# Kernel tuning notes

Hardware: AMD Instinct MI355X
Metric: run time of the kernel (lower is better)

The kernel has to match this reference:

```python
import jax, jax.numpy as jnp
import numpy as np

K, M, C, P = 3, 64, 1, 7
EPS = 1e-16


def _conv_c(x, w, transpose=False):
    """Complex 2D conv (stride 1, SAME padding) decomposed into 4 real convs.
    x: complex [B,Cin,H,W]; w: complex torch-layout weight.
    transpose=True emulates nn.ConvTranspose2d(M,C,P,stride=1,padding=(P-1)//2):
    weight layout (in=M, out=C, P, P), spatially flipped kernel.
    """
    xr, xi = jnp.real(x), jnp.imag(x)
    wr, wi = jnp.real(w), jnp.imag(w)
    if transpose:
        wr = jnp.flip(wr, (2, 3))
        wi = jnp.flip(wi, (2, 3))
        dn = ('NCHW', 'IOHW', 'NCHW')
    else:
        dn = ('NCHW', 'OIHW', 'NCHW')
    f = lambda a, b: jax.lax.conv_general_dilated(
        a, b, window_strides=(1, 1), padding='SAME', dimension_numbers=dn)
    return jax.lax.complex(f(xr, wr) - f(xi, wi), f(xr, wi) + f(xi, wr))


def _st_complex(x, t):
    """Complex soft-threshold: x * relu(|x| - t) / (|x| + eps)."""
    a = jnp.abs(x)
    return x * (jax.nn.relu(a - t) / (a + EPS))


def setup_inputs() -> dict:
    key = jax.random.key(0)
    ks = jax.random.split(key, 7)
    B, H, W = 4, 256, 256
    wscale = 1.0 / np.sqrt(2.0 * M * P * P)  # keep unrolled loop stable
    return {
        'y_re': jax.random.normal(ks[0], (B, C, H, W), jnp.float32),
        'y_im': jax.random.normal(ks[1], (B, C, H, W), jnp.float32),
        'Aw_re': jax.random.normal(ks[2], (K, M, C, P, P), jnp.float32) * wscale,
        'Aw_im': jax.random.normal(ks[3], (K, M, C, P, P), jnp.float32) * wscale,
        'Bw_re': jax.random.normal(ks[4], (K, M, C, P, P), jnp.float32) * wscale,
        'Bw_im': jax.random.normal(ks[5], (K, M, C, P, P), jnp.float32) * wscale,
        't': jax.random.uniform(ks[6], (K, 2, M, 1, 1), jnp.float32) * 0.01,
    }


def reference(y_re, y_im, Aw_re, Aw_im, Bw_re, Bw_im, t):
    y = jax.lax.complex(y_re, y_im)
    Aw = jax.lax.complex(Aw_re, Aw_im)   # [K,M,C,P,P], Conv2d weights
    Bw = jax.lax.complex(Bw_re, Bw_im)   # [K,M,C,P,P], ConvTranspose2d weights

    # pre_process (stride=1, mask=1): mean-subtract, no padding
    mean = jnp.mean(y, axis=(1, 2, 3), keepdims=True)
    yp = y - mean

    # _lista_core with sigma=None, adaptive=False => c=0, threshold = t[k,0]
    z = _st_complex(_conv_c(yp, Aw[0]), t[0, 0])  # [B,M,H,W] complex
    for k in range(1, K):
        r = _conv_c(z, Bw[k], transpose=True) - yp  # mask == 1
        z = z - _conv_c(r, Aw[k])
        z = _st_complex(z, t[k, 0])

    # decode: D = B[0]; post_process adds mean back
    xhat = _conv_c(z, Bw[0], transpose=True) + mean
    return xhat, z
```

## Files before the change

### kernel.cpp

```cpp
#include <hip/hip_runtime.h>

#define Hh 256
#define Ww 256
#define NB 4
#define NM 64
#define KP 7
#define HW (Hh*Ww)
#define NX (NB*HW)
#define NZQ ((size_t)NB*NM*HW)
#define PT 32
#define TW2 38
#define LDS2 40
#define NST 6
#define NTAP (3*NM*49)
#define NSPL 4

typedef unsigned short u16;
typedef unsigned int u32;

__device__ __forceinline__ float bf2f(u16 u) {
  union { u32 i; float f; } c; c.i = ((u32)u) << 16; return c.f;
}
__device__ __forceinline__ u16 f2bf(float f) {
  union { float f; u32 i; } c; c.f = f;
  return (u16)((c.i + 0x7FFFu + ((c.i >> 16) & 1u)) >> 16);
}
__device__ __forceinline__ ushort2 packbf(float x, float y) {
  return make_ushort2(f2bf(x), f2bf(y));
}

__device__ __forceinline__ u32 packh(float x, float y) {
  union { u32 u; _Float16 h[2]; } c;
  c.h[0] = (_Float16)x; c.h[1] = (_Float16)y;
  return c.u;
}
__device__ __forceinline__ float2 unpackh(u32 v) {
  union { u32 u; _Float16 h[2]; } c; c.u = v;
  return make_float2((float)c.h[0], (float)c.h[1]);
}
__device__ __forceinline__ u16 h2bf(u16 hraw) {
  union { u16 u; _Float16 h; } c; c.u = hraw;
  return f2bf((float)c.h);
}

#if __has_builtin(__builtin_amdgcn_fdot2)
typedef _Float16 hf2 __attribute__((ext_vector_type(2)));
__device__ __forceinline__ void cmac2(float& ar, float& ai, u32 v, u32 wre, u32 wim) {
  union { u32 u; hf2 h; } a, b, c;
  a.u = v; b.u = wre; c.u = wim;
  ar = __builtin_amdgcn_fdot2(a.h, b.h, ar, false);
  ai = __builtin_amdgcn_fdot2(a.h, c.h, ai, false);
}
#else
__device__ __forceinline__ void cmac2(float& ar, float& ai, u32 v, u32 wre, u32 wim) {
  float2 a = unpackh(v), b = unpackh(wre), c = unpackh(wim);
  ar = fmaf(a.x, b.x, ar); ar = fmaf(a.y, b.y, ar);
  ai = fmaf(a.x, c.x, ai); ai = fmaf(a.y, c.y, ai);
}
#endif

__global__ __launch_bounds__(256) void wprep_kernel(
    const float* __restrict__ Awre, const float* __restrict__ Awim,
    const float* __restrict__ Bwre, const float* __restrict__ Bwim,
    uint2* __restrict__ wA, uint2* __restrict__ wB) {
  int i = blockIdx.x*256 + threadIdx.x;
  if (i < NTAP) {
    float wr = Awre[i], wi = Awim[i];
    wA[i] = make_uint2(packh(wr, -wi), packh(wi, wr));
    wr = Bwre[i]; wi = Bwim[i];
    wB[i] = make_uint2(packh(wr, -wi), packh(wi, wr));
  }
}

__global__ __launch_bounds__(256) void mean_stage1(
    const float* __restrict__ yre, const float* __restrict__ yim,
    float2* __restrict__ part) {
  int blk = blockIdx.x;
  int b = blk >> 6, chunk = blk & 63;
  int tid = threadIdx.x;
  int base = b*HW + chunk*1024;
  float sr = 0.f, si = 0.f;
  #pragma unroll
  for (int j = 0; j < 4; ++j) {
    sr += yre[base + tid + j*256];
    si += yim[base + tid + j*256];
  }
  #pragma unroll
  for (int off = 32; off > 0; off >>= 1) {
    sr += __shfl_down(sr, off);
    si += __shfl_down(si, off);
  }
  __shared__ float2 red[4];
  if ((tid & 63) == 0) red[tid >> 6] = make_float2(sr, si);
  __syncthreads();
  if (tid == 0) {
    float2 a = red[0], b2 = red[1], c = red[2], d = red[3];
    part[blk] = make_float2(a.x + b2.x + c.x + d.x, a.y + b2.y + c.y + d.y);
  }
}

__global__ __launch_bounds__(256) void mean_stage2(
    const float2* __restrict__ part, float2* __restrict__ mean) {
  int tid = threadIdx.x;
  int b = tid >> 6, lane = tid & 63;
  float2 v = part[b*64 + lane];
  float sr = v.x, si = v.y;
  #pragma unroll
  for (int off = 32; off > 0; off >>= 1) {
    sr += __shfl_down(sr, off);
    si += __shfl_down(si, off);
  }
  if (lane == 0) mean[b] = make_float2(sr / (float)HW, si / (float)HW);
}

__global__ __launch_bounds__(256) void conv_first_kernel(
    const float* __restrict__ yre, const float* __restrict__ yim,
    const float2* __restrict__ mean,
    const uint2* __restrict__ wA,
    const float* __restrict__ t, u32* __restrict__ z) {
  int tid = threadIdx.x;
  int blk = blockIdx.x;
  int ms  = blk & 3;
  int txi = (blk >> 2) & 7, tyi = (blk >> 5) & 7, b = (blk >> 8) & 3;
  int ty0 = tyi*PT, tx0 = txi*PT;
  int thy = tid >> 4, thx = tid & 15;

  __shared__ u32 tile[TW2][LDS2];
  float2 mb = mean[b];
  const float* re = yre + b*HW;
  const float* im = yim + b*HW;
  for (int i = tid; i < TW2*TW2; i += 256) {
    int rr = i / TW2, cc = i - rr*TW2;
    int gy = ty0 - 3 + rr, gx = tx0 - 3 + cc;
    u32 v = 0;
    if ((unsigned)gy < Hh && (unsigned)gx < Ww) {
      int o = gy*Ww + gx;
      v = packh(re[o] - mb.x, im[o] - mb.y);
    }
    tile[rr][cc] = v;
  }
  __syncthreads();

  u32* zb = z + ((size_t)b*NM << 16);
  int m0 = ms*16;
  #pragma unroll 1
  for (int mm = 0; mm < 16; mm += 4) {
    int m = m0 + mm;
    const uint2* w0p = wA + m*49;
    float ar[4][4], ai[4][4];
    #pragma unroll
    for (int c = 0; c < 4; ++c)
      #pragma unroll
      for (int p = 0; p < 4; ++p) { ar[c][p] = 0.f; ai[c][p] = 0.f; }
    #pragma unroll
    for (int ky = 0; ky < KP; ++ky) {
      #pragma unroll
      for (int kx = 0; kx < KP; ++kx) {
        int wo = ky*KP + kx;
        uint2 w0 = w0p[wo], w1 = w0p[49 + wo], w2 = w0p[98 + wo], w3 = w0p[147 + wo];
        #pragma unroll
        for (int dy = 0; dy < 2; ++dy) {
          #pragma unroll
          for (int dx = 0; dx < 2; ++dx) {
            u32 v = tile[thy + dy*16 + ky][thx + dx*16 + kx];
            int p = dy*2 + dx;
            cmac2(ar[0][p], ai[0][p], v, w0.x, w0.y);
            cmac2(ar[1][p], ai[1][p], v, w1.x, w1.y);
            cmac2(ar[2][p], ai[2][p], v, w2.x, w2.y);
            cmac2(ar[3][p], ai[3][p], v, w3.x, w3.y);
          }
        }
      }
    }
    #pragma unroll
    for (int c = 0; c < 4; ++c) {
      float tc = t[m + c];
      #pragma unroll
      for (int dy = 0; dy < 2; ++dy) {
        #pragma unroll
        for (int dx = 0; dx < 2; ++dx) {
          int p = dy*2 + dx;
          size_t o = (size_t)(ty0 + thy + dy*16)*Ww + tx0 + thx + dx*16;
          float a0 = sqrtf(ar[c][p]*ar[c][p] + ai[c][p]*ai[c][p]);
          float f0 = fmaxf(a0 - tc, 0.f) / (a0 + 1e-16f);
          zb[((size_t)(m + c) << 16) + o] = packh(ar[c][p]*f0, ai[c][p]*f0);
        }
      }
    }
  }
}

__global__ __launch_bounds__(256) void convT_part_kernel(
    const u32* __restrict__ z,
    const uint2* __restrict__ wB,
    int k, float2* __restrict__ rpart) {
  int tid = threadIdx.x;
  int blk = blockIdx.x;
  int s   = blk & 3;
  int txi = (blk >> 2) & 7, tyi = (blk >> 5) & 7, b = (blk >> 8) & 3;
  int ty0 = tyi*PT, tx0 = txi*PT;
  int thy = tid >> 4, thx = tid & 15;

  __shared__ uint2 tile[TW2][LDS2];

  int srr[NST], scc[NST], soff[NST];
  bool sok[NST], sin[NST];
  #pragma unroll
  for (int j = 0; j < NST; ++j) {
    int i = tid + j*256;
    sin[j] = i < TW2*TW2;
    int rr = sin[j] ? i / TW2 : 0;
    int cc = sin[j] ? i - rr*TW2 : 0;
    int gy = ty0 - 3 + rr, gx = tx0 - 3 + cc;
    sok[j] = sin[j] && (unsigned)gy < Hh && (unsigned)gx < Ww;
    srr[j] = rr; scc[j] = cc;
    soff[j] = sok[j] ? gy*Ww + gx : 0;
  }

  const u32* zb = z + ((size_t)b*NM << 16);
  int m0 = s*16;

  float ar[4] = {0.f,0.f,0.f,0.f}, ai[4] = {0.f,0.f,0.f,0.f};
  #pragma unroll 1
  for (int q = 0; q < 8; ++q) {
    int m = m0 + 2*q;
    if (q) __syncthreads();
    {
      const u32* za = zb + ((size_t)m << 16);
      const u32* zc = zb + ((size_t)(m + 1) << 16);
      #pragma unroll
      for (int j = 0; j < NST; ++j)
        if (sin[j]) tile[srr[j]][scc[j]] =
          make_uint2(sok[j] ? za[soff[j]] : 0u, sok[j] ? zc[soff[j]] : 0u);
    }
    __syncthreads();

    const uint2* w0p = wB + (k*NM + m)*49;
    const uint2* w1p = w0p + 49;
    #pragma unroll
    for (int ky = 0; ky < KP; ++ky) {
      #pragma unroll
      for (int kx = 0; kx < KP; ++kx) {
        int wo = ky*KP + kx;
        uint2 wa = w0p[wo], wb = w1p[wo];
        #pragma unroll
        for (int dy = 0; dy < 2; ++dy) {
          #pragma unroll
          for (int dx = 0; dx < 2; ++dx) {
            uint2 v = tile[thy + dy*16 + 6 - ky][thx + dx*16 + 6 - kx];
            int p = dy*2 + dx;
            cmac2(ar[p], ai[p], v.x, wa.x, wa.y);
            cmac2(ar[p], ai[p], v.y, wb.x, wb.y);
          }
        }
      }
    }
  }

  float2* rp = rpart + (size_t)s*NB*HW + (size_t)b*HW;
  #pragma unroll
  for (int dy = 0; dy < 2; ++dy) {
    #pragma unroll
    for (int dx = 0; dx < 2; ++dx) {
      int p = dy*2 + dx;
      int o = (ty0 + thy + dy*16)*Ww + tx0 + thx + dx*16;
      rp[o] = make_float2(ar[p], ai[p]);
    }
  }
}

__global__ __launch_bounds__(256) void conv_update_kernel(
    const float2* __restrict__ rpart,
    const float* __restrict__ yre, const float* __restrict__ yim,
    const float2* __restrict__ mean,
    const uint2* __restrict__ wA,
    const float* __restrict__ t, int k, u32* __restrict__ z) {
  int tid = threadIdx.x;
  int blk = blockIdx.x;
  int ms  = blk & 3;
  int txi = (blk >> 2) & 7, tyi = (blk >> 5) & 7, b = (blk >> 8) & 3;
  int ty0 = tyi*PT, tx0 = txi*PT;
  int thy = tid >> 4, thx = tid & 15;

  __shared__ u32 tile[TW2][LDS2];
  float2 mb = mean[b];
  for (int i = tid; i < TW2*TW2; i += 256) {
    int rr = i / TW2, cc = i - rr*TW2;
    int gy = ty0 - 3 + rr, gx = tx0 - 3 + cc;
    u32 v = 0;
    if ((unsigned)gy < Hh && (unsigned)gx < Ww) {
      int o = b*HW + gy*Ww + gx;
      float2 p0 = rpart[o];
      float2 p1 = rpart[(size_t)NB*HW + o];
      float2 p2 = rpart[(size_t)2*NB*HW + o];
      float2 p3 = rpart[(size_t)3*NB*HW + o];
      v = packh(p0.x + p1.x + p2.x + p3.x - (yre[o] - mb.x),
                p0.y + p1.y + p2.y + p3.y - (yim[o] - mb.y));
    }
    tile[rr][cc] = v;
  }
  __syncthreads();

  const float* tw = t + k*2*NM;
  u32* zb = z + ((size_t)b*NM << 16);
  int m0 = ms*16;
  #pragma unroll 1
  for (int mm = 0; mm < 16; mm += 4) {
    int m = m0 + mm;
    const uint2* w0p = wA + (k*NM + m)*49;
    float ar[4][4], ai[4][4];
    #pragma unroll
    for (int c = 0; c < 4; ++c)
      #pragma unroll
      for (int p = 0; p < 4; ++p) { ar[c][p] = 0.f; ai[c][p] = 0.f; }
    #pragma unroll
    for (int ky = 0; ky < KP; ++ky) {
      #pragma unroll
      for (int kx = 0; kx < KP; ++kx) {
        int wo = ky*KP + kx;
        uint2 w0 = w0p[wo], w1 = w0p[49 + wo], w2 = w0p[98 + wo], w3 = w0p[147 + wo];
        #pragma unroll
        for (int dy = 0; dy < 2; ++dy) {
          #pragma unroll
          for (int dx = 0; dx < 2; ++dx) {
            u32 v = tile[thy + dy*16 + ky][thx + dx*16 + kx];
            int p = dy*2 + dx;
            cmac2(ar[0][p], ai[0][p], v, w0.x, w0.y);
            cmac2(ar[1][p], ai[1][p], v, w1.x, w1.y);
            cmac2(ar[2][p], ai[2][p], v, w2.x, w2.y);
            cmac2(ar[3][p], ai[3][p], v, w3.x, w3.y);
          }
        }
      }
    }
    #pragma unroll
    for (int c = 0; c < 4; ++c) {
      float tc = tw[m + c];
      #pragma unroll
      for (int dy = 0; dy < 2; ++dy) {
        #pragma unroll
        for (int dx = 0; dx < 2; ++dx) {
          int p = dy*2 + dx;
          size_t o = (size_t)(ty0 + thy + dy*16)*Ww + tx0 + thx + dx*16;
          size_t q0 = ((size_t)(m + c) << 16) + o;
          float2 z0 = unpackh(zb[q0]);
          float zr0 = z0.x - ar[c][p], zi0 = z0.y - ai[c][p];
          float a0 = sqrtf(zr0*zr0 + zi0*zi0);
          float f0 = fmaxf(a0 - tc, 0.f) / (a0 + 1e-16f);
          zb[q0] = packh(zr0*f0, zi0*f0);
        }
      }
    }
  }
}

__global__ __launch_bounds__(256) void xreduce_kernel(
    const float2* __restrict__ xpart,
    const float2* __restrict__ mean, ushort2* __restrict__ xws) {
  int p = blockIdx.x*256 + threadIdx.x;
  int b = p >> 16;
  float2 mb = mean[b];
  float2 a0 = xpart[p];
  float2 a1 = xpart[(size_t)NB*HW + p];
  float2 a2 = xpart[(size_t)2*NB*HW + p];
  float2 a3 = xpart[(size_t)3*NB*HW + p];
  xws[p] = packbf(a0.x + a1.x + a2.x + a3.x + mb.x,
                  a0.y + a1.y + a2.y + a3.y + mb.y);
}

__global__ __launch_bounds__(256) void emit_kernel(
    const ushort2* __restrict__ xws, const u32* __restrict__ zws,
    u16* __restrict__ out16) {
  size_t idx = (size_t)blockIdx.x*256 + threadIdx.x;
  ushort2* out2 = (ushort2*)out16;
  if (idx < (size_t)NX) {
    int p = (int)idx;
    ushort2 xp = xws[p];
    u16 nxt = (p + 1 < NX) ? xws[p + 1].x
                           : h2bf((u16)(zws[0] & 0xffffu));
    out2[p + 1] = make_ushort2(xp.y, nxt);
    if (p == 0) out16[1] = xp.x;
  } else {
    size_t q = idx - (size_t)NX;
    u32 zq = zws[q];
    u16 zim = h2bf((u16)(zq >> 16));
    if (q + 1 < NZQ) {
      u16 zre_next = h2bf((u16)(zws[q + 1] & 0xffffu));
      out2[(size_t)262145 + q] = make_ushort2(zim, zre_next);
    } else {
      out16[(size_t)2*NX + 2*NZQ] = zim;
    }
  }
}

extern "C" void kernel_launch(void* const* d_in, const int* in_sizes, int n_in,
                              void* d_out, int out_size, void* d_ws, size_t ws_size,
                              hipStream_t stream) {
  const float* yre  = (const float*)d_in[0];
  const float* yim  = (const float*)d_in[1];
  const float* Awre = (const float*)d_in[2];
  const float* Awim = (const float*)d_in[3];
  const float* Bwre = (const float*)d_in[4];
  const float* Bwim = (const float*)d_in[5];
  const float* t    = (const float*)d_in[6];

  u32*     zws = (u32*)d_ws;
  ushort2* xws = (ushort2*)((char*)d_ws + (size_t)67108864);

  char* ob = (char*)d_out;
  float2* rpart = (float2*)ob;
  float2* xpart = (float2*)(ob + 8388608);
  float2* mean  = (float2*)(ob + 16777216);
  float2* part  = (float2*)(ob + 16777280);
  uint2*  wA    = (uint2*)(ob + 17825792);
  uint2*  wB    = (uint2*)(ob + 18874368);

  wprep_kernel<<<(NTAP + 255)/256, 256, 0, stream>>>(Awre, Awim, Bwre, Bwim, wA, wB);
  mean_stage1<<<256, 256, 0, stream>>>(yre, yim, part);
  mean_stage2<<<1, 256, 0, stream>>>(part, mean);

  dim3 grid1k(NB * (Hh/PT) * (Ww/PT) * NSPL);
  conv_first_kernel<<<grid1k, 256, 0, stream>>>(yre, yim, mean, wA, t, zws);
  for (int k = 1; k < 3; ++k) {
    convT_part_kernel<<<grid1k, 256, 0, stream>>>(zws, wB, k, rpart);
    conv_update_kernel<<<grid1k, 256, 0, stream>>>(rpart, yre, yim, mean, wA, t, k, zws);
  }
  convT_part_kernel<<<grid1k, 256, 0, stream>>>(zws, wB, 0, xpart);
  xreduce_kernel<<<NX/256, 256, 0, stream>>>(xpart, mean, xws);

  size_t total = (size_t)NX + NZQ;
  emit_kernel<<<(unsigned)(total/256), 256, 0, stream>>>(xws, zws, (u16*)d_out);
}
```

Measured before the change: 537.7 us.

## Stage four channels per LDS tile in convT and pre-fold residual partials

convT_part now loads four z channels per shared-memory tile as uint4, which halves the number of tile reloads and barriers and widens each LDS read. A new rfold_kernel reduces the four residual partials and subtracts y minus mean once per pixel into a packed buffer. Before, each of the four channel-split blocks repeated that reduction over its halo. This adds a kernel launch and an extra global round trip, and doubles the LDS tile size, which may reduce occupancy.

```diff
diff --git a/kernel.cpp b/kernel.cpp
--- a/kernel.cpp
+++ b/kernel.cpp
@@ -201,7 +201,7 @@
   int ty0 = tyi*PT, tx0 = txi*PT;
   int thy = tid >> 4, thx = tid & 15;
 
-  __shared__ uint2 tile[TW2][LDS2];
+  __shared__ uint4 tile[TW2][LDS2];
 
   int srr[NST], scc[NST], soff[NST];
   bool sok[NST], sin[NST];
@@ -222,35 +222,39 @@
 
   float ar[4] = {0.f,0.f,0.f,0.f}, ai[4] = {0.f,0.f,0.f,0.f};
   #pragma unroll 1
-  for (int q = 0; q < 8; ++q) {
-    int m = m0 + 2*q;
+  for (int q = 0; q < 4; ++q) {
+    int m = m0 + 4*q;
     if (q) __syncthreads();
     {
-      const u32* za = zb + ((size_t)m << 16);
-      const u32* zc = zb + ((size_t)(m + 1) << 16);
+      const u32* z0 = zb + ((size_t)m << 16);
+      const u32* z1 = zb + ((size_t)(m + 1) << 16);
+      const u32* z2 = zb + ((size_t)(m + 2) << 16);
+      const u32* z3 = zb + ((size_t)(m + 3) << 16);
       #pragma unroll
       for (int j = 0; j < NST; ++j)
-        if (sin[j]) tile[srr[j]][scc[j]] =
-          make_uint2(sok[j] ? za[soff[j]] : 0u, sok[j] ? zc[soff[j]] : 0u);
+        if (sin[j]) tile[srr[j]][scc[j]] = make_uint4(
+          sok[j] ? z0[soff[j]] : 0u, sok[j] ? z1[soff[j]] : 0u,
+          sok[j] ? z2[soff[j]] : 0u, sok[j] ? z3[soff[j]] : 0u);
     }
     __syncthreads();
 
     const uint2* w0p = wB + (k*NM + m)*49;
-    const uint2* w1p = w0p + 49;
     #pragma unroll
     for (int ky = 0; ky < KP; ++ky) {
       #pragma unroll
       for (int kx = 0; kx < KP; ++kx) {
         int wo = ky*KP + kx;
-        uint2 wa = w0p[wo], wb = w1p[wo];
+        uint2 wa = w0p[wo], wb = w0p[49 + wo], wc = w0p[98 + wo], wd = w0p[147 + wo];
         #pragma unroll
         for (int dy = 0; dy < 2; ++dy) {
           #pragma unroll
           for (int dx = 0; dx < 2; ++dx) {
-            uint2 v = tile[thy + dy*16 + 6 - ky][thx + dx*16 + 6 - kx];
+            uint4 v = tile[thy + dy*16 + 6 - ky][thx + dx*16 + 6 - kx];
             int p = dy*2 + dx;
             cmac2(ar[p], ai[p], v.x, wa.x, wa.y);
             cmac2(ar[p], ai[p], v.y, wb.x, wb.y);
+            cmac2(ar[p], ai[p], v.z, wc.x, wc.y);
+            cmac2(ar[p], ai[p], v.w, wd.x, wd.y);
           }
         }
       }
@@ -269,10 +273,23 @@
   }
 }
 
-__global__ __launch_bounds__(256) void conv_update_kernel(
+__global__ __launch_bounds__(256) void rfold_kernel(
     const float2* __restrict__ rpart,
     const float* __restrict__ yre, const float* __restrict__ yim,
-    const float2* __restrict__ mean,
+    const float2* __restrict__ mean, u32* __restrict__ rq) {
+  int p = blockIdx.x*256 + threadIdx.x;
+  int b = p >> 16;
+  float2 mb = mean[b];
+  float2 p0 = rpart[p];
+  float2 p1 = rpart[(size_t)NB*HW + p];
+  float2 p2 = rpart[(size_t)2*NB*HW + p];
+  float2 p3 = rpart[(size_t)3*NB*HW + p];
+  rq[p] = packh(p0.x + p1.x + p2.x + p3.x - (yre[p] - mb.x),
+                p0.y + p1.y + p2.y + p3.y - (yim[p] - mb.y));
+}
+
+__global__ __launch_bounds__(256) void conv_update_kernel(
+    const u32* __restrict__ rq,
     const uint2* __restrict__ wA,
     const float* __restrict__ t, int k, u32* __restrict__ z) {
   int tid = threadIdx.x;
@@ -283,20 +300,12 @@
   int thy = tid >> 4, thx = tid & 15;
 
   __shared__ u32 tile[TW2][LDS2];
-  float2 mb = mean[b];
+  const u32* rb = rq + b*HW;
   for (int i = tid; i < TW2*TW2; i += 256) {
     int rr = i / TW2, cc = i - rr*TW2;
     int gy = ty0 - 3 + rr, gx = tx0 - 3 + cc;
     u32 v = 0;
-    if ((unsigned)gy < Hh && (unsigned)gx < Ww) {
-      int o = b*HW + gy*Ww + gx;
-      float2 p0 = rpart[o];
-      float2 p1 = rpart[(size_t)NB*HW + o];
-      float2 p2 = rpart[(size_t)2*NB*HW + o];
-      float2 p3 = rpart[(size_t)3*NB*HW + o];
-      v = packh(p0.x + p1.x + p2.x + p3.x - (yre[o] - mb.x),
-                p0.y + p1.y + p2.y + p3.y - (yim[o] - mb.y));
-    }
+    if ((unsigned)gy < Hh && (unsigned)gx < Ww) v = rb[gy*Ww + gx];
     tile[rr][cc] = v;
   }
   __syncthreads();
@@ -414,6 +423,7 @@
   float2* part  = (float2*)(ob + 16777280);
   uint2*  wA    = (uint2*)(ob + 17825792);
   uint2*  wB    = (uint2*)(ob + 18874368);
+  u32*    rq    = (u32*)(ob + 19922944);
 
   wprep_kernel<<<(NTAP + 255)/256, 256, 0, stream>>>(Awre, Awim, Bwre, Bwim, wA, wB);
   mean_stage1<<<256, 256, 0, stream>>>(yre, yim, part);
@@ -423,7 +433,8 @@
   conv_first_kernel<<<grid1k, 256, 0, stream>>>(yre, yim, mean, wA, t, zws);
   for (int k = 1; k < 3; ++k) {
     convT_part_kernel<<<grid1k, 256, 0, stream>>>(zws, wB, k, rpart);
-    conv_update_kernel<<<grid1k, 256, 0, stream>>>(rpart, yre, yim, mean, wA, t, k, zws);
+    rfold_kernel<<<NX/256, 256, 0, stream>>>(rpart, yre, yim, mean, rq);
+    conv_update_kernel<<<grid1k, 256, 0, stream>>>(rq, wA, t, k, zws);
   }
   convT_part_kernel<<<grid1k, 256, 0, stream>>>(zws, wB, 0, xpart);
   xreduce_kernel<<<NX/256, 256, 0, stream>>>(xpart, mean, xws);
```

New measurement: 520.0 us. 3.3% less time.
